# Kernel optimization log

Hardware: AMD Instinct MI355X
Metric: run time of the kernel (lower is better)

The kernel has to match this reference:

```python
import jax, jax.numpy as jnp
import numpy as np
from jax.scipy.special import logsumexp

EPS = 1e-6
SINKHORN_ITERS = 8
TEMPERATURE = 1.0


def sinkhorn(logits):
    # log(clamp(t, min=eps)) / temperature, then alternating row/col log-normalization
    t = jnp.log(jnp.clip(logits, EPS)) / TEMPERATURE
    for _ in range(SINKHORN_ITERS):
        t = t - logsumexp(t, axis=-2, keepdims=True)  # over tokens n
        t = t - logsumexp(t, axis=-1, keepdims=True)  # over experts e
    return jnp.exp(t)


def setup_inputs() -> dict:
    key = jax.random.key(0)
    k1, k2, k3 = jax.random.split(key, 3)
    b, n, d, e, h = 4, 4096, 1024, 8, 1
    x = jax.random.normal(k1, (b, n, d), dtype=jnp.float32)
    gate_w = jax.random.normal(k2, (h, d, e), dtype=jnp.float32)  # to_gate_weight
    experts = jax.random.normal(k3, (e, d, d), dtype=jnp.float32) * 0.02  # expert weight tensor [e, i, o]
    return {"x": x, "gate_w": gate_w, "experts": experts}


def reference(x, gate_w, experts):
    b, n, d = x.shape
    h, _, e = gate_w.shape
    m = n // e  # tokens_per_expert

    xh = x[:, None]  # b 1 n d  (single-headed path)

    # gate logits: b h n e
    gate_logits = jnp.einsum('bhnd,hde->bhne', xh, gate_w)

    # competitive sinkhorn gates (eval mode, no gumbel noise)
    gates = sinkhorn(gate_logits)

    # topk over token dim (dim=-2) with k = tokens_per_expert
    g = jnp.swapaxes(gates, -1, -2)          # b h e n
    gv, idx = jax.lax.top_k(g, m)            # b h e m
    gate_values = jnp.swapaxes(gv, -1, -2)   # b h m e
    routed_indices = jnp.swapaxes(idx, -1, -2)  # b h m e

    # eval + competitive -> hard gates
    hard_gates = (gate_values > 0.5).astype(x.dtype)  # b h m e

    # gather routed tokens: routed[b,h,m,e,d] = x[b,h,idx[b,h,m,e],d]
    bi = jnp.arange(b)[:, None, None, None]
    hi = jnp.arange(h)[None, :, None, None]
    routed = xh[bi, hi, routed_indices]  # b h m e d

    # per-expert GEMM, vectorized over experts: experts [e,i,o] -> [e,h,i,o]
    experts4 = experts[:, None, :, :]
    out = jnp.einsum('bhmei,ehio->bhmeo', routed, experts4)  # b h m e o

    # weight by gates
    out = out * hard_gates[..., None]

    # scatter back (set semantics, as in einx set_at)
    y = jnp.zeros_like(xh).at[bi, hi, routed_indices].set(out)  # b h n d
    return y[:, 0]  # b n d
```

## Files before the change

kernel.cpp:

```cpp
#include <hip/hip_runtime.h>
#include <hip/hip_bf16.h>
#include <stdint.h>

#define BB 4
#define NN 4096
#define DD 1024
#define EE 8
#define MM 512
#define BN (BB*NN)

#define SBLK 32
#define SPB  8
#define SROWS 512

#define FRONT_GATE 512
#define FRONT_CONV 2048

typedef __bf16 bf16x8 __attribute__((ext_vector_type(8)));
typedef float  floatx4 __attribute__((ext_vector_type(4)));

typedef const __attribute__((address_space(1))) void* gptr_t;
typedef __attribute__((address_space(3))) void* lptr_t;

__device__ __forceinline__ unsigned short f2bf(float f) {
    union { float f; unsigned u; } v; v.f = f;
    unsigned r = v.u + 0x7fffu + ((v.u >> 16) & 1u);
    return (unsigned short)(r >> 16);
}

__device__ __forceinline__ float gate_reduce8(const float acc[8], int lane) {
    float k1[4];
#pragma unroll
    for (int e = 0; e < 4; e++) {
        float a = acc[e]     + __shfl_xor(acc[e],     1, 64);
        float b = acc[e + 4] + __shfl_xor(acc[e + 4], 1, 64);
        k1[e] = (lane & 1) ? b : a;
    }
    float k2[2];
#pragma unroll
    for (int e = 0; e < 2; e++) {
        float a = k1[e]     + __shfl_xor(k1[e],     2, 64);
        float b = k1[e + 2] + __shfl_xor(k1[e + 2], 2, 64);
        k2[e] = (lane & 2) ? b : a;
    }
    float a = k2[0] + __shfl_xor(k2[0], 4, 64);
    float b = k2[1] + __shfl_xor(k2[1], 4, 64);
    float v = (lane & 4) ? b : a;
    v += __shfl_xor(v, 8, 64);
    v += __shfl_xor(v, 16, 64);
    v += __shfl_xor(v, 32, 64);
    return v;
}

#define OFF_GATES   0u
#define OFF_COUNTS  655360u
#define OFF_LISTS   655616u
#define OFF_FLAGS   721152u
#define OFF_PART    737536u
#define OFF_KEYS    753920u
#define OFF_XBF     1802496u
#define OFF_EXPT    35356928u
#define WS_NEEDED   52134144u

__global__ __launch_bounds__(256, 2) void gate_kernel(const float* __restrict__ x,
                                                      const float* __restrict__ gw,
                                                      float* __restrict__ tmat,
                                                      unsigned short* __restrict__ xbf,
                                                      int* __restrict__ counts,
                                                      unsigned* __restrict__ flags) {
    int bid = blockIdx.x;
    int tid = threadIdx.x;
    if (bid >= FRONT_GATE) {
        if (tid < 32) counts[tid] = 0;
        for (int i = tid; i < 4096; i += 256) flags[i] = 0u;
        return;
    }
    int wave = tid >> 6, lane = tid & 63;
    float4 g0[4][4], g1[4][4];
#pragma unroll
    for (int j = 0; j < 4; j++)
#pragma unroll
        for (int r = 0; r < 4; r++) {
            const float4* p = (const float4*)(gw + (size_t)(j * 256 + lane * 4 + r) * 8);
            g0[j][r] = p[0];
            g1[j][r] = p[1];
        }
    int tok0 = (bid * 4 + wave) * 8;
    int exp_id = ((lane & 1) << 2) | (lane & 2) | ((lane & 4) >> 2);

    float4 xa[4], xc[4], na[4], nc[4];
    {
        const float4* xr = (const float4*)(x + (size_t)tok0 * DD);
#pragma unroll
        for (int j = 0; j < 4; j++) xa[j] = xr[j * 64 + lane];
#pragma unroll
        for (int j = 0; j < 4; j++) xc[j] = xr[256 + j * 64 + lane];
    }
#pragma unroll
    for (int tt = 0; tt < 8; tt += 2) {
        int tokA = tok0 + tt, tokB = tokA + 1;
        if (tt < 6) {
            const float4* xrn = (const float4*)(x + (size_t)(tokA + 2) * DD);
#pragma unroll
            for (int j = 0; j < 4; j++) na[j] = xrn[j * 64 + lane];
#pragma unroll
            for (int j = 0; j < 4; j++) nc[j] = xrn[256 + j * 64 + lane];
        }
        if (xbf) {
#pragma unroll
            for (int j = 0; j < 4; j++) {
                ushort4 o;
                o.x = f2bf(xa[j].x); o.y = f2bf(xa[j].y); o.z = f2bf(xa[j].z); o.w = f2bf(xa[j].w);
                ((ushort4*)(xbf + (size_t)tokA * DD))[j * 64 + lane] = o;
            }
#pragma unroll
            for (int j = 0; j < 4; j++) {
                ushort4 o;
                o.x = f2bf(xc[j].x); o.y = f2bf(xc[j].y); o.z = f2bf(xc[j].z); o.w = f2bf(xc[j].w);
                ((ushort4*)(xbf + (size_t)tokB * DD))[j * 64 + lane] = o;
            }
        }
        float accA[8] = {0.f, 0.f, 0.f, 0.f, 0.f, 0.f, 0.f, 0.f};
        float accB[8] = {0.f, 0.f, 0.f, 0.f, 0.f, 0.f, 0.f, 0.f};
#pragma unroll
        for (int j = 0; j < 4; j++) {
            accA[0] += xa[j].x * g0[j][0].x + xa[j].y * g0[j][1].x + xa[j].z * g0[j][2].x + xa[j].w * g0[j][3].x;
            accA[1] += xa[j].x * g0[j][0].y + xa[j].y * g0[j][1].y + xa[j].z * g0[j][2].y + xa[j].w * g0[j][3].y;
            accA[2] += xa[j].x * g0[j][0].z + xa[j].y * g0[j][1].z + xa[j].z * g0[j][2].z + xa[j].w * g0[j][3].z;
            accA[3] += xa[j].x * g0[j][0].w + xa[j].y * g0[j][1].w + xa[j].z * g0[j][2].w + xa[j].w * g0[j][3].w;
            accA[4] += xa[j].x * g1[j][0].x + xa[j].y * g1[j][1].x + xa[j].z * g1[j][2].x + xa[j].w * g1[j][3].x;
            accA[5] += xa[j].x * g1[j][0].y + xa[j].y * g1[j][1].y + xa[j].z * g1[j][2].y + xa[j].w * g1[j][3].y;
            accA[6] += xa[j].x * g1[j][0].z + xa[j].y * g1[j][1].z + xa[j].z * g1[j][2].z + xa[j].w * g1[j][3].z;
            accA[7] += xa[j].x * g1[j][0].w + xa[j].y * g1[j][1].w + xa[j].z * g1[j][2].w + xa[j].w * g1[j][3].w;
            accB[0] += xc[j].x * g0[j][0].x + xc[j].y * g0[j][1].x + xc[j].z * g0[j][2].x + xc[j].w * g0[j][3].x;
            accB[1] += xc[j].x * g0[j][0].y + xc[j].y * g0[j][1].y + xc[j].z * g0[j][2].y + xc[j].w * g0[j][3].y;
            accB[2] += xc[j].x * g0[j][0].z + xc[j].y * g0[j][1].z + xc[j].z * g0[j][2].z + xc[j].w * g0[j][3].z;
            accB[3] += xc[j].x * g0[j][0].w + xc[j].y * g0[j][1].w + xc[j].z * g0[j][2].w + xc[j].w * g0[j][3].w;
            accB[4] += xc[j].x * g1[j][0].x + xc[j].y * g1[j][1].x + xc[j].z * g1[j][2].x + xc[j].w * g1[j][3].x;
            accB[5] += xc[j].x * g1[j][0].y + xc[j].y * g1[j][1].y + xc[j].z * g1[j][2].y + xc[j].w * g1[j][3].y;
            accB[6] += xc[j].x * g1[j][0].z + xc[j].y * g1[j][1].z + xc[j].z * g1[j][2].z + xc[j].w * g1[j][3].z;
            accB[7] += xc[j].x * g1[j][0].w + xc[j].y * g1[j][1].w + xc[j].z * g1[j][2].w + xc[j].w * g1[j][3].w;
        }
        float vA = gate_reduce8(accA, lane);
        float vB = gate_reduce8(accB, lane);
        if (lane < 8) {
            tmat[(size_t)tokA * EE + exp_id] = logf(fmaxf(vA, 1e-6f));
            tmat[(size_t)tokB * EE + exp_id] = logf(fmaxf(vB, 1e-6f));
        }
        if (tt < 6) {
#pragma unroll
            for (int j = 0; j < 4; j++) { xa[j] = na[j]; xc[j] = nc[j]; }
        }
    }
}

__global__ void sinkhorn_conv(const float* __restrict__ tmat,
                              float* __restrict__ part,
                              unsigned* __restrict__ flags,
                              unsigned long long* __restrict__ keys,
                              int* __restrict__ rank,
                              const float* __restrict__ E,
                              unsigned short* __restrict__ expt) {
    __shared__ float tile[64][65];
    __shared__ float red[8][8];
    __shared__ float bcm[8];
    int g = blockIdx.x;
    int tid = threadIdx.x;

    if (g >= SBLK) {
        if (!expt) return;
        int cb = g - SBLK;
        int e = cb >> 8, t = cb & 255;
        int k0 = (t >> 4) * 64, c0 = (t & 15) * 64;
        int r = tid >> 3, c8 = (tid & 7) * 8;
        const float* src = E + ((size_t)e * DD + k0 + r) * DD + c0 + c8;
        float4 v0 = *(const float4*)src;
        float4 v1 = *(const float4*)(src + 4);
        tile[r][c8 + 0] = v0.x; tile[r][c8 + 1] = v0.y; tile[r][c8 + 2] = v0.z; tile[r][c8 + 3] = v0.w;
        tile[r][c8 + 4] = v1.x; tile[r][c8 + 5] = v1.y; tile[r][c8 + 6] = v1.z; tile[r][c8 + 7] = v1.w;
        __syncthreads();
        int cc = tid >> 3, kk8 = (tid & 7) * 8;
        ushort4 o0, o1;
        o0.x = f2bf(tile[kk8 + 0][cc]); o0.y = f2bf(tile[kk8 + 1][cc]);
        o0.z = f2bf(tile[kk8 + 2][cc]); o0.w = f2bf(tile[kk8 + 3][cc]);
        o1.x = f2bf(tile[kk8 + 4][cc]); o1.y = f2bf(tile[kk8 + 5][cc]);
        o1.z = f2bf(tile[kk8 + 6][cc]); o1.w = f2bf(tile[kk8 + 7][cc]);
        unsigned short* dst = expt + ((size_t)e * DD + c0 + cc) * DD + k0 + kk8;
        *(ushort4*)dst = o0;
        *(ushort4*)(dst + 4) = o1;
        return;
    }

    int b = g >> 3, sl = g & 7;
    int wave = tid >> 6, lane = tid & 63;
    int row = sl * SROWS + tid;
    const float* tr = tmat + ((size_t)b * NN + row) * EE;
    float tv[EE];
#pragma unroll
    for (int e = 0; e < EE; e++) tv[e] = tr[e];

    for (int it = 0; it < 8; it++) {
#pragma unroll
        for (int e = 0; e < EE; e++) {
            float s = expf(tv[e]);
            for (int off = 32; off > 0; off >>= 1) s += __shfl_down(s, off, 64);
            if (lane == 0) red[wave][e] = s;
        }
        __syncthreads();
        if (tid == 0) {
            float* pm = part + (size_t)(it * 32 + b * 8 + sl) * 16;
#pragma unroll
            for (int e = 0; e < EE; e++) {
                float s = 0.f;
#pragma unroll
                for (int w = 0; w < 8; w++) s += red[w][e];
                __hip_atomic_store(&pm[e], s, __ATOMIC_RELAXED, __HIP_MEMORY_SCOPE_AGENT);
            }
            __hip_atomic_store(&flags[(size_t)(it * 32 + b * 8 + sl) * 16], 1u,
                               __ATOMIC_RELEASE, __HIP_MEMORY_SCOPE_AGENT);
        }
        if (tid < 8) {
            const unsigned* f = flags + (size_t)(it * 32 + b * 8 + tid) * 16;
            while (__hip_atomic_load(f, __ATOMIC_ACQUIRE, __HIP_MEMORY_SCOPE_AGENT) == 0u)
                __builtin_amdgcn_s_sleep(1);
        }
        __syncthreads();
        if (tid < 8) {
            const float* pb = part + (size_t)(it * 32 + b * 8) * 16;
            float s = 0.f;
#pragma unroll
            for (int p = 0; p < SPB; p++)
                s += __hip_atomic_load(&pb[p * 16 + tid], __ATOMIC_RELAXED, __HIP_MEMORY_SCOPE_AGENT);
            bcm[tid] = logf(s);
        }
        __syncthreads();
#pragma unroll
        for (int e = 0; e < EE; e++) tv[e] -= bcm[e];
        {
            float s = 0.f;
#pragma unroll
            for (int e = 0; e < EE; e++) s += expf(tv[e]);
            float lse = logf(s);
#pragma unroll
            for (int e = 0; e < EE; e++) tv[e] -= lse;
        }
    }
#pragma unroll
    for (int e = 0; e < EE; e++) {
        unsigned fb = __float_as_uint(expf(tv[e]));
        keys[(size_t)(b * EE + e) * NN + row] =
            ((unsigned long long)fb << 32) | (unsigned)(~row);
    }
    {
        int4* rz = (int4*)(rank + (size_t)b * EE * NN) + (size_t)sl * (EE * NN / 8 / 4);
        int4 z4 = make_int4(0, 0, 0, 0);
        rz[tid * 2 + 0] = z4;
        rz[tid * 2 + 1] = z4;
    }
}

__global__ __launch_bounds__(256) void rank_count_kernel(const unsigned long long* __restrict__ keys,
                                                         int* __restrict__ rank) {
    int be = blockIdx.y;
    int tid = threadIdx.x;
    int t = blockIdx.x * 256 + tid;
    const unsigned long long* kcol = keys + (size_t)be * NN;
    unsigned long long my = kcol[t];
    const unsigned long long* ks = kcol + (size_t)blockIdx.z * (NN / 4);

    int c0 = 0, c1 = 0, c2 = 0, c3 = 0;
    for (int j = 0; j < NN / 4; j += 16) {
#pragma unroll
        for (int i = 0; i < 16; i += 4) {
            c0 += (int)(ks[j + i + 0] > my);
            c1 += (int)(ks[j + i + 1] > my);
            c2 += (int)(ks[j + i + 2] > my);
            c3 += (int)(ks[j + i + 3] > my);
        }
    }
    atomicAdd(&rank[(size_t)be * NN + t], (c0 + c1) + (c2 + c3));
}

__global__ __launch_bounds__(256) void build_zero_kernel(const unsigned long long* __restrict__ keys,
                                                         const int* __restrict__ rank,
                                                         int* __restrict__ counts,
                                                         int* __restrict__ lists,
                                                         float* __restrict__ y) {
    __shared__ int act_s[64];
    int base = blockIdx.x * 64;
    int tid = threadIdx.x;
    if (tid < 64) {
        int i = base + tid;
        int b = i >> 12, tok = i & 4095;
        int wmax = -1;
#pragma unroll
        for (int e = 0; e < EE; e++) {
            int r = rank[(size_t)(b * 8 + e) * NN + tok];
            if (r < MM) {
                int w = r * 8 + e;
                wmax = wmax > w ? wmax : w;
            }
        }
        int active = 0;
        if (wmax >= 0) {
            int ew = wmax & 7;
            unsigned hi = (unsigned)(keys[(size_t)(b * 8 + ew) * NN + tok] >> 32);
            if (__uint_as_float(hi) > 0.5f) {
                int p = atomicAdd(&counts[b * 8 + ew], 1);
                lists[(b * 8 + ew) * MM + p] = tok;
                active = 1;
            }
        }
        act_s[tid] = active;
    }
    __syncthreads();
    float4 z = make_float4(0.f, 0.f, 0.f, 0.f);
    for (int r = 0; r < 64; r++) {
        if (!act_s[r])
            ((float4*)(y + (size_t)(base + r) * DD))[tid] = z;
    }
}

__global__ __launch_bounds__(256) void expert_gemm_mfma(const unsigned short* __restrict__ xbf,
                                                        const unsigned short* __restrict__ expt,
                                                        const int* __restrict__ counts,
                                                        const int* __restrict__ lists,
                                                        float* __restrict__ y) {
    int be = blockIdx.z;
    int b = be >> 3, e = be & 7;
    int cnt = counts[be];
    int row0 = blockIdx.y * 64;
    if (row0 >= cnt) return;
    int col0 = blockIdx.x * 128;

    __shared__ unsigned short As[64 * 32];
    __shared__ unsigned short Bs[128 * 32];
    __shared__ int toks[64];

    int tid = threadIdx.x;
    int wave = tid >> 6, lane = tid & 63;
    int m16 = lane & 15, quad = lane >> 4;
    int wave_m = wave >> 1, wave_n = wave & 1;

    if (tid < 64) {
        int r = row0 + tid;
        toks[tid] = lists[be * MM + (r < cnt ? r : cnt - 1)];
    }

    int r0 = tid >> 2;
    int ch = tid & 3;

    const unsigned short* xb = xbf + (size_t)b * NN * DD;
    const unsigned short* Eb = expt + (size_t)e * DD * DD;

    floatx4 acc[2][4];
#pragma unroll
    for (int i = 0; i < 2; i++)
#pragma unroll
        for (int j = 0; j < 4; j++) acc[i][j] = (floatx4)0.f;

    for (int k0 = 0; k0 < DD; k0 += 32) {
        __syncthreads();
        {
            const unsigned short* gA  = xb + (size_t)toks[r0] * DD + k0 + ch * 8;
            const unsigned short* gB0 = Eb + (size_t)(col0 + r0) * DD + k0 + ch * 8;
            const unsigned short* gB1 = Eb + (size_t)(col0 + 64 + r0) * DD + k0 + ch * 8;
            __builtin_amdgcn_global_load_lds((gptr_t)gA,  (lptr_t)(As + (size_t)tid * 8), 16, 0, 0);
            __builtin_amdgcn_global_load_lds((gptr_t)gB0, (lptr_t)(Bs + (size_t)tid * 8), 16, 0, 0);
            __builtin_amdgcn_global_load_lds((gptr_t)gB1, (lptr_t)(Bs + 64 * 32 + (size_t)tid * 8), 16, 0, 0);
        }
        __syncthreads();
        bf16x8 af[2], bfr[4];
#pragma unroll
        for (int i = 0; i < 2; i++)
            af[i] = *(const bf16x8*)&As[(wave_m * 32 + i * 16 + m16) * 32 + quad * 8];
#pragma unroll
        for (int j = 0; j < 4; j++)
            bfr[j] = *(const bf16x8*)&Bs[(wave_n * 64 + j * 16 + m16) * 32 + quad * 8];
#pragma unroll
        for (int i = 0; i < 2; i++)
#pragma unroll
            for (int j = 0; j < 4; j++)
                acc[i][j] = __builtin_amdgcn_mfma_f32_16x16x32_bf16(af[i], bfr[j], acc[i][j], 0, 0, 0);
    }

#pragma unroll
    for (int i = 0; i < 2; i++) {
#pragma unroll
        for (int r = 0; r < 4; r++) {
            int lr = wave_m * 32 + i * 16 + quad * 4 + r;
            if (row0 + lr < cnt) {
                int tok = toks[lr];
                float* yr = y + ((size_t)b * NN + tok) * DD + col0 + wave_n * 64 + m16;
#pragma unroll
                for (int j = 0; j < 4; j++) yr[j * 16] = acc[i][j][r];
            }
        }
    }
}

__global__ __launch_bounds__(256) void expert_gemm_kernel(const float* __restrict__ x,
                                                          const float* __restrict__ experts,
                                                          const int* __restrict__ counts,
                                                          const int* __restrict__ lists,
                                                          float* __restrict__ y) {
    int be = blockIdx.z;
    int b = be >> 3, e = be & 7;
    int cnt = counts[be];
    int row0 = blockIdx.y * 64;
    if (row0 >= cnt) return;
    int col0 = blockIdx.x * 64;
    __shared__ float As2[16][68];
    __shared__ float Bs2[16][68];
    __shared__ int toks[64];
    int tid = threadIdx.x;
    if (tid < 64) {
        int r = row0 + tid;
        toks[tid] = (r < cnt) ? lists[be * MM + r] : -1;
    }
    __syncthreads();
    int tx = tid & 15, ty = tid >> 4;
    int ar = tid >> 2;
    int ak = (tid & 3) * 4;
    int bk = tid >> 4;
    int bc4 = (tid & 15) * 4;
    int atok = toks[ar];
    const float* xb = x + (size_t)b * NN * DD;
    const float* Eb = experts + (size_t)e * DD * DD + col0;
    float acc[4][4] = {};
    for (int k0 = 0; k0 < DD; k0 += 16) {
        float4 av;
        if (atok >= 0) av = *(const float4*)(xb + (size_t)atok * DD + k0 + ak);
        else av = make_float4(0.f, 0.f, 0.f, 0.f);
        float4 bv = *(const float4*)(Eb + (size_t)(k0 + bk) * DD + bc4);
        __syncthreads();
        As2[ak + 0][ar] = av.x; As2[ak + 1][ar] = av.y; As2[ak + 2][ar] = av.z; As2[ak + 3][ar] = av.w;
        *(float4*)&Bs2[bk][bc4] = bv;
        __syncthreads();
#pragma unroll
        for (int kk = 0; kk < 16; kk++) {
            float4 a = *(const float4*)&As2[kk][ty * 4];
            float4 bb = *(const float4*)&Bs2[kk][tx * 4];
            acc[0][0] += a.x * bb.x; acc[0][1] += a.x * bb.y; acc[0][2] += a.x * bb.z; acc[0][3] += a.x * bb.w;
            acc[1][0] += a.y * bb.x; acc[1][1] += a.y * bb.y; acc[1][2] += a.y * bb.z; acc[1][3] += a.y * bb.w;
            acc[2][0] += a.z * bb.x; acc[2][1] += a.z * bb.y; acc[2][2] += a.z * bb.z; acc[2][3] += a.z * bb.w;
            acc[3][0] += a.w * bb.x; acc[3][1] += a.w * bb.y; acc[3][2] += a.w * bb.z; acc[3][3] += a.w * bb.w;
        }
    }
#pragma unroll
    for (int i = 0; i < 4; i++) {
        int rl = ty * 4 + i;
        if (row0 + rl < cnt) {
            int tok = toks[rl];
            float4 o = make_float4(acc[i][0], acc[i][1], acc[i][2], acc[i][3]);
            *(float4*)(y + ((size_t)b * NN + tok) * DD + col0 + tx * 4) = o;
        }
    }
}

extern "C" void kernel_launch(void* const* d_in, const int* in_sizes, int n_in,
                              void* d_out, int out_size, void* d_ws, size_t ws_size,
                              hipStream_t stream) {
    const float* x       = (const float*)d_in[0];
    const float* gw      = (const float*)d_in[1];
    const float* experts = (const float*)d_in[2];
    float* y = (float*)d_out;

    char* ws = (char*)d_ws;
    float*    gates    = (float*)(ws + OFF_GATES);
    int*      rank     = (int*)(ws + OFF_GATES);
    int*      counts   = (int*)(ws + OFF_COUNTS);
    int*      lists    = (int*)(ws + OFF_LISTS);
    unsigned* flags    = (unsigned*)(ws + OFF_FLAGS);
    float*    part     = (float*)(ws + OFF_PART);
    unsigned long long* keys = (unsigned long long*)(ws + OFF_KEYS);
    bool big = ws_size >= WS_NEEDED;
    unsigned short* xbf  = big ? (unsigned short*)(ws + OFF_XBF)  : nullptr;
    unsigned short* expt = big ? (unsigned short*)(ws + OFF_EXPT) : nullptr;

    gate_kernel<<<FRONT_GATE + 1, 256, 0, stream>>>(x, gw, gates, xbf, counts, flags);
    sinkhorn_conv<<<SBLK + FRONT_CONV, 512, 0, stream>>>(gates, part, flags, keys, rank,
                                                         experts, expt);
    rank_count_kernel<<<dim3(16, 32, 4), 256, 0, stream>>>(keys, rank);
    build_zero_kernel<<<256, 256, 0, stream>>>(keys, rank, counts, lists, y);
    if (big)
        expert_gemm_mfma<<<dim3(8, 8, BB * EE), 256, 0, stream>>>(xbf, expt, counts, lists, y);
    else
        expert_gemm_kernel<<<dim3(16, 8, BB * EE), 256, 0, stream>>>(x, experts, counts, lists, y);
}
```

Before: 280.5 us.

## Run Sinkhorn per batch in a single block, removing inter-block flag synchronization

Sinkhorn normalization previously split each batch across 8 blocks, which exchanged partial column sums through global memory with release/acquire flags and spin-waits on every iteration. Now one 512-thread block handles a whole batch, holding 8 rows per thread in registers. Column sums are reduced with a transposing shuffle reduction and shared memory, so no grid-level handshake is needed. The cost is a far less parallel Sinkhorn phase (4 blocks instead of 32), higher register use, and removal of the flag-clearing work.

```diff
diff --git a/kernel.cpp b/kernel.cpp
--- a/kernel.cpp
+++ b/kernel.cpp
@@ -9,12 +9,9 @@
 #define MM 512
 #define BN (BB*NN)
 
-#define SBLK 32
-#define SPB  8
-#define SROWS 512
-
 #define FRONT_GATE 512
 #define FRONT_CONV 2048
+#define SKBLK 4
 
 typedef __bf16 bf16x8 __attribute__((ext_vector_type(8)));
 typedef float  floatx4 __attribute__((ext_vector_type(4)));
@@ -55,8 +52,6 @@
 #define OFF_GATES   0u
 #define OFF_COUNTS  655360u
 #define OFF_LISTS   655616u
-#define OFF_FLAGS   721152u
-#define OFF_PART    737536u
 #define OFF_KEYS    753920u
 #define OFF_XBF     1802496u
 #define OFF_EXPT    35356928u
@@ -66,13 +61,11 @@
                                                       const float* __restrict__ gw,
                                                       float* __restrict__ tmat,
                                                       unsigned short* __restrict__ xbf,
-                                                      int* __restrict__ counts,
-                                                      unsigned* __restrict__ flags) {
+                                                      int* __restrict__ counts) {
     int bid = blockIdx.x;
     int tid = threadIdx.x;
     if (bid >= FRONT_GATE) {
         if (tid < 32) counts[tid] = 0;
-        for (int i = tid; i < 4096; i += 256) flags[i] = 0u;
         return;
     }
     int wave = tid >> 6, lane = tid & 63;
@@ -154,22 +147,20 @@
     }
 }
 
-__global__ void sinkhorn_conv(const float* __restrict__ tmat,
-                              float* __restrict__ part,
-                              unsigned* __restrict__ flags,
-                              unsigned long long* __restrict__ keys,
-                              int* __restrict__ rank,
-                              const float* __restrict__ E,
-                              unsigned short* __restrict__ expt) {
+__global__ __launch_bounds__(512) void sinkhorn_conv(const float* __restrict__ tmat,
+                                                     unsigned long long* __restrict__ keys,
+                                                     int* __restrict__ rank,
+                                                     const float* __restrict__ E,
+                                                     unsigned short* __restrict__ expt) {
     __shared__ float tile[64][65];
     __shared__ float red[8][8];
     __shared__ float bcm[8];
     int g = blockIdx.x;
     int tid = threadIdx.x;
 
-    if (g >= SBLK) {
+    if (g >= SKBLK) {
         if (!expt) return;
-        int cb = g - SBLK;
+        int cb = g - SKBLK;
         int e = cb >> 8, t = cb & 255;
         int k0 = (t >> 4) * 64, c0 = (t & 15) * 64;
         int r = tid >> 3, c8 = (tid & 7) * 8;
@@ -191,71 +182,68 @@
         return;
     }
 
-    int b = g >> 3, sl = g & 7;
+    int b = g;
     int wave = tid >> 6, lane = tid & 63;
-    int row = sl * SROWS + tid;
-    const float* tr = tmat + ((size_t)b * NN + row) * EE;
-    float tv[EE];
-#pragma unroll
-    for (int e = 0; e < EE; e++) tv[e] = tr[e];
+    const float* tb = tmat + (size_t)b * NN * EE;
+    float tv[8][8];
+#pragma unroll
+    for (int k = 0; k < 8; k++) {
+        const float4* p = (const float4*)(tb + (size_t)(k * 512 + tid) * EE);
+        float4 v0 = p[0], v1 = p[1];
+        tv[k][0] = v0.x; tv[k][1] = v0.y; tv[k][2] = v0.z; tv[k][3] = v0.w;
+        tv[k][4] = v1.x; tv[k][5] = v1.y; tv[k][6] = v1.z; tv[k][7] = v1.w;
+    }
 
     for (int it = 0; it < 8; it++) {
-#pragma unroll
-        for (int e = 0; e < EE; e++) {
-            float s = expf(tv[e]);
-            for (int off = 32; off > 0; off >>= 1) s += __shfl_down(s, off, 64);
-            if (lane == 0) red[wave][e] = s;
-        }
-        __syncthreads();
-        if (tid == 0) {
-            float* pm = part + (size_t)(it * 32 + b * 8 + sl) * 16;
-#pragma unroll
-            for (int e = 0; e < EE; e++) {
-                float s = 0.f;
-#pragma unroll
-                for (int w = 0; w < 8; w++) s += red[w][e];
-                __hip_atomic_store(&pm[e], s, __ATOMIC_RELAXED, __HIP_MEMORY_SCOPE_AGENT);
-            }
-            __hip_atomic_store(&flags[(size_t)(it * 32 + b * 8 + sl) * 16], 1u,
-                               __ATOMIC_RELEASE, __HIP_MEMORY_SCOPE_AGENT);
-        }
+        float ls[8];
+#pragma unroll
+        for (int e = 0; e < 8; e++) {
+            float s = 0.f;
+#pragma unroll
+            for (int k = 0; k < 8; k++) s += expf(tv[k][e]);
+            ls[e] = s;
+        }
+        float r8 = gate_reduce8(ls, lane);
+        if (lane < 8) {
+            int eid = ((lane & 1) << 2) | (lane & 2) | ((lane & 4) >> 2);
+            red[wave][eid] = r8;
+        }
+        __syncthreads();
         if (tid < 8) {
-            const unsigned* f = flags + (size_t)(it * 32 + b * 8 + tid) * 16;
-            while (__hip_atomic_load(f, __ATOMIC_ACQUIRE, __HIP_MEMORY_SCOPE_AGENT) == 0u)
-                __builtin_amdgcn_s_sleep(1);
-        }
-        __syncthreads();
-        if (tid < 8) {
-            const float* pb = part + (size_t)(it * 32 + b * 8) * 16;
             float s = 0.f;
 #pragma unroll
-            for (int p = 0; p < SPB; p++)
-                s += __hip_atomic_load(&pb[p * 16 + tid], __ATOMIC_RELAXED, __HIP_MEMORY_SCOPE_AGENT);
+            for (int w = 0; w < 8; w++) s += red[w][tid];
             bcm[tid] = logf(s);
         }
         __syncthreads();
-#pragma unroll
-        for (int e = 0; e < EE; e++) tv[e] -= bcm[e];
-        {
+        float bl[8];
+#pragma unroll
+        for (int e = 0; e < 8; e++) bl[e] = bcm[e];
+#pragma unroll
+        for (int k = 0; k < 8; k++) {
             float s = 0.f;
 #pragma unroll
-            for (int e = 0; e < EE; e++) s += expf(tv[e]);
+            for (int e = 0; e < 8; e++) { tv[k][e] -= bl[e]; s += expf(tv[k][e]); }
             float lse = logf(s);
 #pragma unroll
-            for (int e = 0; e < EE; e++) tv[e] -= lse;
-        }
-    }
-#pragma unroll
-    for (int e = 0; e < EE; e++) {
-        unsigned fb = __float_as_uint(expf(tv[e]));
-        keys[(size_t)(b * EE + e) * NN + row] =
-            ((unsigned long long)fb << 32) | (unsigned)(~row);
+            for (int e = 0; e < 8; e++) tv[k][e] -= lse;
+        }
+    }
+#pragma unroll
+    for (int k = 0; k < 8; k++) {
+        int row = k * 512 + tid;
+#pragma unroll
+        for (int e = 0; e < 8; e++) {
+            unsigned fb = __float_as_uint(expf(tv[k][e]));
+            keys[(size_t)(b * EE + e) * NN + row] =
+                ((unsigned long long)fb << 32) | (unsigned)(~row);
+        }
     }
     {
-        int4* rz = (int4*)(rank + (size_t)b * EE * NN) + (size_t)sl * (EE * NN / 8 / 4);
+        int4* rz = (int4*)(rank + (size_t)b * EE * NN);
         int4 z4 = make_int4(0, 0, 0, 0);
-        rz[tid * 2 + 0] = z4;
-        rz[tid * 2 + 1] = z4;
+#pragma unroll
+        for (int q = 0; q < 16; q++) rz[q * 512 + tid] = z4;
     }
 }
 
@@ -471,16 +459,14 @@
     int*      rank     = (int*)(ws + OFF_GATES);
     int*      counts   = (int*)(ws + OFF_COUNTS);
     int*      lists    = (int*)(ws + OFF_LISTS);
-    unsigned* flags    = (unsigned*)(ws + OFF_FLAGS);
-    float*    part     = (float*)(ws + OFF_PART);
     unsigned long long* keys = (unsigned long long*)(ws + OFF_KEYS);
     bool big = ws_size >= WS_NEEDED;
     unsigned short* xbf  = big ? (unsigned short*)(ws + OFF_XBF)  : nullptr;
     unsigned short* expt = big ? (unsigned short*)(ws + OFF_EXPT) : nullptr;
 
-    gate_kernel<<<FRONT_GATE + 1, 256, 0, stream>>>(x, gw, gates, xbf, counts, flags);
-    sinkhorn_conv<<<SBLK + FRONT_CONV, 512, 0, stream>>>(gates, part, flags, keys, rank,
-                                                         experts, expt);
+    gate_kernel<<<FRONT_GATE + 1, 256, 0, stream>>>(x, gw, gates, xbf, counts);
+    sinkhorn_conv<<<SKBLK + FRONT_CONV, 512, 0, stream>>>(gates, keys, rank,
+                                                          experts, expt);
     rank_count_kernel<<<dim3(16, 32, 4), 256, 0, stream>>>(keys, rank);
     build_zero_kernel<<<256, 256, 0, stream>>>(keys, rank, counts, lists, y);
     if (big)
```

Result: slower. 299.3 us (+6.7%).
